# Kernel tuning notes

Hardware: AMD Instinct MI355X
Metric: run time of the kernel (lower is better)

The kernel has to match this reference:

```python
import jax, jax.numpy as jnp
import numpy as np

N_NODES = 100000
N_EDGES = 1250000
D = 64


def setup_inputs() -> dict:
    key = jax.random.key(0)
    k0, k1, k2, k3, k4 = jax.random.split(key, 5)
    feat = jax.random.normal(k0, (N_NODES, D), dtype=jnp.float32)
    src = jax.random.randint(k1, (N_EDGES,), 0, N_NODES)
    dst = jax.random.randint(k2, (N_EDGES,), 0, N_NODES)
    # GIN apply_func: Linear(D, D) -> ReLU -> Linear(D, D)
    scale = 1.0 / np.sqrt(D)
    W1 = jax.random.uniform(k3, (D, D), dtype=jnp.float32, minval=-scale, maxval=scale)
    b1 = jnp.zeros((D,), dtype=jnp.float32)
    W2 = jax.random.uniform(k4, (D, D), dtype=jnp.float32, minval=-scale, maxval=scale)
    b2 = jnp.zeros((D,), dtype=jnp.float32)
    eps = jnp.zeros((1,), dtype=jnp.float32)  # learnable eps, init 0
    return {"feat": feat, "W1": W1, "b1": b1, "W2": W2, "b2": b2,
            "eps": eps, "src": src, "dst": dst}


def reference(feat, W1, b1, W2, b2, eps, src, dst):
    # copy_u + sum reduce: gather source features per edge, scatter-add to dst
    msgs = feat[src]                                   # [E, D]
    neigh = jax.ops.segment_sum(msgs, dst, num_segments=feat.shape[0])  # [N, D]
    rst = (1.0 + eps) * feat + neigh                   # combine
    # apply_func (f_Theta): 2-layer MLP
    h = jax.nn.relu(rst @ W1 + b1)
    out = h @ W2 + b2
    return out
```

## Files before the change

### kernel.cpp

```cpp
#include <hip/hip_runtime.h>
#include <hip/hip_bf16.h>

#define N_NODES 100000
#define N_EDGES 1250000
#define DIM 64
#define NB 782
#define NCHUNK 512
#define CHUNK 2442
#define MAXE 4096

typedef __attribute__((ext_vector_type(8))) short short8;
typedef __attribute__((ext_vector_type(8))) __bf16 bf16x8;
typedef __attribute__((ext_vector_type(4))) float f32x4;

static __device__ __forceinline__ short f2bf(float f) {
    union { float f; unsigned u; } v; v.f = f;
    unsigned r = (v.u + 0x7fffu + ((v.u >> 16) & 1u)) >> 16;
    return (short)r;
}
static __device__ __forceinline__ float bfu2f(unsigned u) {
    union { unsigned u; float f; } v; v.u = u << 16; return v.f;
}
static __device__ __forceinline__ float bfs2f(short s) {
    union { unsigned u; float f; } v; v.u = ((unsigned)(unsigned short)s) << 16; return v.f;
}
static __device__ __forceinline__ int wave_scan(int v, int lane) {
#pragma unroll
    for (int off = 1; off < 64; off <<= 1) {
        int n = __shfl_up(v, off, 64);
        if (lane >= off) v += n;
    }
    return v;
}

__global__ __launch_bounds__(256) void prologue(const float* __restrict__ feat,
                                                short* __restrict__ featbf,
                                                const float* __restrict__ W1,
                                                const float* __restrict__ W2,
                                                short* __restrict__ wf,
                                                int basePrep) {
    int blk = blockIdx.x;
    if (blk < basePrep) {
        int i = (blk * 256 + threadIdx.x) * 8;
        float4 a = *(const float4*)(feat + i);
        float4 b = *(const float4*)(feat + i + 4);
        short8 t;
        t[0] = f2bf(a.x); t[1] = f2bf(a.y); t[2] = f2bf(a.z); t[3] = f2bf(a.w);
        t[4] = f2bf(b.x); t[5] = f2bf(b.y); t[6] = f2bf(b.z); t[7] = f2bf(b.w);
        *(short8*)(featbf + i) = t;
    } else {
        int idx = (blk - basePrep) * 256 + threadIdx.x;
        int layer = idx >> 12;
        int fi = idx & 4095;
        int fragidx = fi >> 9;
        int lane = (fi >> 3) & 63;
        int jj = fi & 7;
        int ct = fragidx >> 1, kt = fragidx & 1;
        int k = kt * 32 + (lane >> 4) * 8 + jj;
        int j = ct * 16 + (lane & 15);
        const float* W = layer ? W2 : W1;
        wf[idx] = f2bf(W[k * DIM + j]);
    }
}

__global__ __launch_bounds__(512) void partition3(const int* __restrict__ src,
                                                  const int* __restrict__ dst,
                                                  int* __restrict__ offs_gT,
                                                  int* __restrict__ edgebuf) {
    __shared__ int cnt[NB];
    __shared__ int lcur[NB];
    __shared__ int wsum[8];
    __shared__ int estage[CHUNK];

    int c = blockIdx.x;
    int t = threadIdx.x;
    int lane = t & 63, wv = t >> 6;
    int base = c * CHUNK;
    int end = base + CHUNK; if (end > N_EDGES) end = N_EDGES;

    for (int b = t; b < NB; b += 512) cnt[b] = 0;
    __syncthreads();
    for (int i = base + t; i < end; i += 512)
        atomicAdd(&cnt[dst[i] >> 7], 1);
    __syncthreads();

    int b0 = 2 * t, b1 = 2 * t + 1;
    int v0 = (b0 < NB) ? cnt[b0] : 0;
    int v1 = (b1 < NB) ? cnt[b1] : 0;
    int isc = wave_scan(v0 + v1, lane);
    if (lane == 63) wsum[wv] = isc;
    __syncthreads();
    if (wv == 0) {
        int s = (lane < 8) ? wsum[lane] : 0;
#pragma unroll
        for (int off = 1; off < 8; off <<= 1) {
            int n = __shfl_up(s, off, 64);
            if (lane >= off) s += n;
        }
        if (lane < 8) wsum[lane] = s;
    }
    __syncthreads();
    int ex = (wv ? wsum[wv - 1] : 0) + isc - (v0 + v1);
    if (b0 < NB) { lcur[b0] = ex;      offs_gT[(size_t)b0 * NCHUNK + c] = ex; }
    if (b1 < NB) { lcur[b1] = ex + v0; offs_gT[(size_t)b1 * NCHUNK + c] = ex + v0; }
    if (t == 511) offs_gT[(size_t)NB * NCHUNK + c] = wsum[7];
    __syncthreads();

    for (int i = base + t; i < end; i += 512) {
        int d = dst[i];
        int p = atomicAdd(&lcur[d >> 7], 1);
        estage[p] = src[i] | ((d & 127) << 17);
    }
    __syncthreads();

    int n = end - base;
    for (int i = t; i < n; i += 512) edgebuf[base + i] = estage[i];
}

template<int BF>
__global__ __launch_bounds__(512) void fused_gather_mlp(const int* __restrict__ offs_gT,
                                                        const int* __restrict__ edgebuf,
                                                        const void* __restrict__ featp,
                                                        const float* __restrict__ feat,
                                                        const short* __restrict__ wf,
                                                        const float* __restrict__ b1,
                                                        const float* __restrict__ b2,
                                                        const float* __restrict__ epsp,
                                                        float* __restrict__ out) {
    __shared__ union {
        struct { int ew[MAXE]; int es[MAXE]; } s;
        float tile[128][66];
    } u;
    __shared__ int cnt[128], offs[128], cur[128];
    __shared__ int slen[NCHUNK], dloc[NCHUNK];
    __shared__ int wsum[8];
    __shared__ int csum[2];

    int b = blockIdx.x;
    int node0 = b << 7;
    int tid = threadIdx.x;
    int lane = tid & 63, wv8 = tid >> 6;
    int c = tid & 15;
    int slot = tid >> 4;

    int s0 = offs_gT[(size_t)b * NCHUNK + tid];
    int myslen = offs_gT[(size_t)(b + 1) * NCHUNK + tid] - s0;
    int isc = wave_scan(myslen, lane);
    if (lane == 63) wsum[wv8] = isc;
    __syncthreads();
    if (wv8 == 0) {
        int s = (lane < 8) ? wsum[lane] : 0;
#pragma unroll
        for (int off = 1; off < 8; off <<= 1) {
            int n = __shfl_up(s, off, 64);
            if (lane >= off) s += n;
        }
        if (lane < 8) wsum[lane] = s;
    }
    __syncthreads();
    int incl = (wv8 ? wsum[wv8 - 1] : 0) + isc;
    dloc[tid] = incl - myslen;
    slen[tid] = myslen;
    int ec = wsum[7];
    __syncthreads();

    float acc[4][4];
#pragma unroll
    for (int g = 0; g < 4; ++g)
#pragma unroll
        for (int j = 0; j < 4; ++j) acc[g][j] = 0.f;

    int c0 = 0;
    while (c0 < NCHUNK) {
        int rbase = dloc[c0];
        int pred = (tid >= c0) && (dloc[tid] + slen[tid] - rbase <= MAXE);
        int nc = __syncthreads_count(pred);
        int c1 = c0 + nc;

        if (tid < 128) cnt[tid] = 0;
        if (tid >= c0 && tid < c1 && myslen > 0) {
            int d0 = dloc[tid] - rbase;
            const int* sp = edgebuf + (size_t)tid * CHUNK + s0;
            for (int i = 0; i < myslen; ++i) u.s.ew[d0 + i] = sp[i];
        }
        __syncthreads();

        int n = ((c1 < NCHUNK) ? dloc[c1] : ec) - rbase;

        for (int i = tid; i < n; i += 512)
            atomicAdd(&cnt[(u.s.ew[i] >> 17) & 127], 1);
        __syncthreads();

        int v_c = (tid < 128) ? cnt[tid] : 0;
        int s_c = 0;
        if (wv8 < 2) {
            s_c = wave_scan(v_c, lane);
            if (lane == 63) csum[wv8] = s_c;
        }
        __syncthreads();
        if (tid < 128) {
            int basec = (wv8 == 1) ? csum[0] : 0;
            int x = basec + s_c - v_c;
            offs[tid] = x;
            cur[tid] = x;
        }
        __syncthreads();

        for (int i = tid; i < n; i += 512) {
            int w = u.s.ew[i];
            int p = atomicAdd(&cur[(w >> 17) & 127], 1);
            u.s.es[p] = w & 0x1FFFF;
        }
        __syncthreads();

#pragma unroll
        for (int g = 0; g < 4; ++g) {
            int ld = g * 32 + slot;
            int e0 = offs[ld], e1 = e0 + cnt[ld];
            int i = e0;
            if (BF) {
                const uint2* fb = (const uint2*)featp;
                for (; i + 7 < e1; i += 8) {
                    uint2 pv[8];
#pragma unroll
                    for (int k = 0; k < 8; ++k) pv[k] = fb[u.s.es[i + k] * 16 + c];
                    float a0 = 0.f, a1 = 0.f, a2 = 0.f, a3 = 0.f;
#pragma unroll
                    for (int k = 0; k < 8; ++k) {
                        a0 += bfu2f(pv[k].x & 0xffffu);
                        a1 += bfu2f(pv[k].x >> 16);
                        a2 += bfu2f(pv[k].y & 0xffffu);
                        a3 += bfu2f(pv[k].y >> 16);
                    }
                    acc[g][0] += a0; acc[g][1] += a1;
                    acc[g][2] += a2; acc[g][3] += a3;
                }
                for (; i + 3 < e1; i += 4) {
                    uint2 pv[4];
#pragma unroll
                    for (int k = 0; k < 4; ++k) pv[k] = fb[u.s.es[i + k] * 16 + c];
#pragma unroll
                    for (int k = 0; k < 4; ++k) {
                        acc[g][0] += bfu2f(pv[k].x & 0xffffu);
                        acc[g][1] += bfu2f(pv[k].x >> 16);
                        acc[g][2] += bfu2f(pv[k].y & 0xffffu);
                        acc[g][3] += bfu2f(pv[k].y >> 16);
                    }
                }
                for (; i < e1; ++i) {
                    uint2 pa = fb[u.s.es[i] * 16 + c];
                    acc[g][0] += bfu2f(pa.x & 0xffffu);
                    acc[g][1] += bfu2f(pa.x >> 16);
                    acc[g][2] += bfu2f(pa.y & 0xffffu);
                    acc[g][3] += bfu2f(pa.y >> 16);
                }
            } else {
                const float4* ff = (const float4*)featp;
                for (; i + 3 < e1; i += 4) {
                    float4 pv[4];
#pragma unroll
                    for (int k = 0; k < 4; ++k) pv[k] = ff[u.s.es[i + k] * 16 + c];
#pragma unroll
                    for (int k = 0; k < 4; ++k) {
                        acc[g][0] += pv[k].x; acc[g][1] += pv[k].y;
                        acc[g][2] += pv[k].z; acc[g][3] += pv[k].w;
                    }
                }
                for (; i < e1; ++i) {
                    float4 qa = ff[u.s.es[i] * 16 + c];
                    acc[g][0] += qa.x; acc[g][1] += qa.y;
                    acc[g][2] += qa.z; acc[g][3] += qa.w;
                }
            }
        }
        __syncthreads();
        c0 = c1;
    }

#pragma unroll
    for (int g = 0; g < 4; ++g) {
        int ld = g * 32 + slot;
#pragma unroll
        for (int j = 0; j < 4; ++j)
            u.tile[ld][c * 4 + j] = acc[g][j];
    }
    __syncthreads();

    int r = lane & 15, gg = lane >> 4;
    int lrow = wv8 * 16 + r;
    int node = node0 + lrow;
    bool valid = node < N_NODES;
    float epsv = 1.0f + epsp[0];

    const short8* w1f8 = (const short8*)(wf);
    const short8* w2f8 = (const short8*)(wf + 4096);

    short8 a[2];
#pragma unroll
    for (int kt = 0; kt < 2; ++kt) {
        float fv[8];
        if (BF) {
            short8 f8 = { 0,0,0,0,0,0,0,0 };
            if (valid) f8 = ((const short8*)featp)[node * 8 + kt * 4 + gg];
#pragma unroll
            for (int jj = 0; jj < 8; ++jj) fv[jj] = bfs2f(f8[jj]);
        } else {
            float4 f0 = { 0,0,0,0 }, f1 = { 0,0,0,0 };
            if (valid) {
                const float* fp = feat + (size_t)node * 64 + kt * 32 + gg * 8;
                f0 = *(const float4*)fp;
                f1 = *(const float4*)(fp + 4);
            }
            fv[0]=f0.x; fv[1]=f0.y; fv[2]=f0.z; fv[3]=f0.w;
            fv[4]=f1.x; fv[5]=f1.y; fv[6]=f1.z; fv[7]=f1.w;
        }
        const float2* tp = (const float2*)&u.tile[lrow][kt * 32 + gg * 8];
        float2 n0 = tp[0], n1 = tp[1], n2 = tp[2], n3 = tp[3];
        float rs[8] = { epsv * fv[0] + n0.x, epsv * fv[1] + n0.y,
                        epsv * fv[2] + n1.x, epsv * fv[3] + n1.y,
                        epsv * fv[4] + n2.x, epsv * fv[5] + n2.y,
                        epsv * fv[6] + n3.x, epsv * fv[7] + n3.y };
        short8 t;
#pragma unroll
        for (int jj = 0; jj < 8; ++jj) t[jj] = f2bf(rs[jj]);
        a[kt] = t;
    }
    __syncthreads();

    f32x4 acc1[4];
#pragma unroll
    for (int ct = 0; ct < 4; ++ct) {
        float bv = b1[ct * 16 + r];
        f32x4 cc = { bv, bv, bv, bv };
        cc = __builtin_amdgcn_mfma_f32_16x16x32_bf16(
                __builtin_bit_cast(bf16x8, a[0]),
                __builtin_bit_cast(bf16x8, w1f8[(ct * 2 + 0) * 64 + lane]),
                cc, 0, 0, 0);
        cc = __builtin_amdgcn_mfma_f32_16x16x32_bf16(
                __builtin_bit_cast(bf16x8, a[1]),
                __builtin_bit_cast(bf16x8, w1f8[(ct * 2 + 1) * 64 + lane]),
                cc, 0, 0, 0);
        acc1[ct] = cc;
    }

#pragma unroll
    for (int ct = 0; ct < 4; ++ct)
#pragma unroll
        for (int i = 0; i < 4; ++i)
            u.tile[wv8 * 16 + gg * 4 + i][ct * 16 + r] = fmaxf(acc1[ct][i], 0.0f);
    __syncthreads();

    short8 a2[2];
#pragma unroll
    for (int kt = 0; kt < 2; ++kt) {
        const float2* hp = (const float2*)&u.tile[wv8 * 16 + r][kt * 32 + gg * 8];
        float2 h0 = hp[0], h1 = hp[1], h2 = hp[2], h3 = hp[3];
        float hs[8] = { h0.x, h0.y, h1.x, h1.y, h2.x, h2.y, h3.x, h3.y };
        short8 t;
#pragma unroll
        for (int jj = 0; jj < 8; ++jj) t[jj] = f2bf(hs[jj]);
        a2[kt] = t;
    }

    f32x4 acc2[4];
#pragma unroll
    for (int ct = 0; ct < 4; ++ct) {
        float bv = b2[ct * 16 + r];
        f32x4 cc = { bv, bv, bv, bv };
        cc = __builtin_amdgcn_mfma_f32_16x16x32_bf16(
                __builtin_bit_cast(bf16x8, a2[0]),
                __builtin_bit_cast(bf16x8, w2f8[(ct * 2 + 0) * 64 + lane]),
                cc, 0, 0, 0);
        cc = __builtin_amdgcn_mfma_f32_16x16x32_bf16(
                __builtin_bit_cast(bf16x8, a2[1]),
                __builtin_bit_cast(bf16x8, w2f8[(ct * 2 + 1) * 64 + lane]),
                cc, 0, 0, 0);
        acc2[ct] = cc;
    }

#pragma unroll
    for (int ct = 0; ct < 4; ++ct)
#pragma unroll
        for (int i = 0; i < 4; ++i) {
            int nrow = node0 + wv8 * 16 + gg * 4 + i;
            if (nrow < N_NODES)
                out[(size_t)nrow * 64 + ct * 16 + r] = acc2[ct][i];
        }
}

__global__ __launch_bounds__(256) void scatter_edges(const float4* __restrict__ feat4,
                                                     const int* __restrict__ src,
                                                     const int* __restrict__ dst,
                                                     float* __restrict__ neigh) {
    int idx = blockIdx.x * 256 + threadIdx.x;
    int e = idx >> 4, c = idx & 15;
    int s = src[e], d = dst[e];
    float4 v = feat4[s * 16 + c];
    float* p = neigh + d * 64 + c * 4;
    unsafeAtomicAdd(p + 0, v.x);
    unsafeAtomicAdd(p + 1, v.y);
    unsafeAtomicAdd(p + 2, v.z);
    unsafeAtomicAdd(p + 3, v.w);
}

__global__ __launch_bounds__(256) void prep_w(const float* __restrict__ W1,
                                              const float* __restrict__ W2,
                                              short* __restrict__ wf) {
    int idx = blockIdx.x * 256 + threadIdx.x;
    int layer = idx >> 12;
    int fi = idx & 4095;
    int fragidx = fi >> 9;
    int lane = (fi >> 3) & 63;
    int jj = fi & 7;
    int ct = fragidx >> 1, kt = fragidx & 1;
    int k = kt * 32 + (lane >> 4) * 8 + jj;
    int j = ct * 16 + (lane & 15);
    const float* W = layer ? W2 : W1;
    wf[idx] = f2bf(W[k * DIM + j]);
}

__global__ __launch_bounds__(256) void gin_mlp(const float* __restrict__ feat,
                                               float* __restrict__ neigh_out,
                                               const short* __restrict__ wf,
                                               const float* __restrict__ b1,
                                               const float* __restrict__ b2,
                                               const float* __restrict__ epsp) {
    __shared__ float hbuf[4][16][66];
    int lane = threadIdx.x & 63;
    int wv = threadIdx.x >> 6;
    int r = lane & 15, g = lane >> 4;
    int row0 = blockIdx.x * 64 + wv * 16;
    int node = row0 + r;
    bool valid = node < N_NODES;
    float epsv = 1.0f + epsp[0];
    const short8* w1f8 = (const short8*)(wf);
    const short8* w2f8 = (const short8*)(wf + 4096);
    short8 a[2];
    if (valid) {
        const float* fp = feat + node * 64 + g * 8;
        const float* np_ = neigh_out + node * 64 + g * 8;
#pragma unroll
        for (int kt = 0; kt < 2; ++kt) {
            float4 f0 = *(const float4*)(fp + kt * 32);
            float4 f1 = *(const float4*)(fp + kt * 32 + 4);
            float4 n0 = *(const float4*)(np_ + kt * 32);
            float4 n1 = *(const float4*)(np_ + kt * 32 + 4);
            float rs[8] = { epsv * f0.x + n0.x, epsv * f0.y + n0.y,
                            epsv * f0.z + n0.z, epsv * f0.w + n0.w,
                            epsv * f1.x + n1.x, epsv * f1.y + n1.y,
                            epsv * f1.z + n1.z, epsv * f1.w + n1.w };
            short8 t;
#pragma unroll
            for (int jj = 0; jj < 8; ++jj) t[jj] = f2bf(rs[jj]);
            a[kt] = t;
        }
    } else {
        short8 z = { 0,0,0,0,0,0,0,0 };
        a[0] = z; a[1] = z;
    }
    f32x4 acc[4];
#pragma unroll
    for (int ct = 0; ct < 4; ++ct) {
        float bv = b1[ct * 16 + r];
        f32x4 c = { bv, bv, bv, bv };
        c = __builtin_amdgcn_mfma_f32_16x16x32_bf16(
                __builtin_bit_cast(bf16x8, a[0]),
                __builtin_bit_cast(bf16x8, w1f8[(ct * 2 + 0) * 64 + lane]), c, 0, 0, 0);
        c = __builtin_amdgcn_mfma_f32_16x16x32_bf16(
                __builtin_bit_cast(bf16x8, a[1]),
                __builtin_bit_cast(bf16x8, w1f8[(ct * 2 + 1) * 64 + lane]), c, 0, 0, 0);
        acc[ct] = c;
    }
#pragma unroll
    for (int ct = 0; ct < 4; ++ct)
#pragma unroll
        for (int i = 0; i < 4; ++i)
            hbuf[wv][g * 4 + i][ct * 16 + r] = fmaxf(acc[ct][i], 0.0f);
    __syncthreads();
    short8 a2[2];
#pragma unroll
    for (int kt = 0; kt < 2; ++kt) {
        const float2* hp = (const float2*)&hbuf[wv][r][kt * 32 + g * 8];
        float2 h0 = hp[0], h1 = hp[1], h2 = hp[2], h3 = hp[3];
        float hs[8] = { h0.x, h0.y, h1.x, h1.y, h2.x, h2.y, h3.x, h3.y };
        short8 t;
#pragma unroll
        for (int jj = 0; jj < 8; ++jj) t[jj] = f2bf(hs[jj]);
        a2[kt] = t;
    }
    f32x4 acc2[4];
#pragma unroll
    for (int ct = 0; ct < 4; ++ct) {
        float bv = b2[ct * 16 + r];
        f32x4 c = { bv, bv, bv, bv };
        c = __builtin_amdgcn_mfma_f32_16x16x32_bf16(
                __builtin_bit_cast(bf16x8, a2[0]),
                __builtin_bit_cast(bf16x8, w2f8[(ct * 2 + 0) * 64 + lane]), c, 0, 0, 0);
        c = __builtin_amdgcn_mfma_f32_16x16x32_bf16(
                __builtin_bit_cast(bf16x8, a2[1]),
                __builtin_bit_cast(bf16x8, w2f8[(ct * 2 + 1) * 64 + lane]), c, 0, 0, 0);
        acc2[ct] = c;
    }
#pragma unroll
    for (int ct = 0; ct < 4; ++ct)
#pragma unroll
        for (int i = 0; i < 4; ++i) {
            int nrow = row0 + g * 4 + i;
            if (nrow < N_NODES)
                neigh_out[nrow * 64 + ct * 16 + r] = acc2[ct][i];
        }
}

extern "C" void kernel_launch(void* const* d_in, const int* in_sizes, int n_in,
                              void* d_out, int out_size, void* d_ws, size_t ws_size,
                              hipStream_t stream) {
    const float* feat = (const float*)d_in[0];
    const float* W1   = (const float*)d_in[1];
    const float* b1   = (const float*)d_in[2];
    const float* W2   = (const float*)d_in[3];
    const float* b2   = (const float*)d_in[4];
    const float* eps  = (const float*)d_in[5];
    const int*   src  = (const int*)d_in[6];
    const int*   dst  = (const int*)d_in[7];
    float* out = (float*)d_out;

    char* ws = (char*)d_ws;
    short* wf = (short*)ws;

    const size_t featbf_bytes = (size_t)N_NODES * DIM * 2;
    const size_t offs_bytes   = (size_t)(NB + 1) * NCHUNK * 4;
    const size_t edge_bytes   = (size_t)NCHUNK * CHUNK * 4;
    const size_t need_mid  = 16384 + offs_bytes + edge_bytes;
    const size_t need_full = need_mid + featbf_bytes;

    if (ws_size >= need_mid) {
        char* p = ws + 16384;
        short* featbf = nullptr;
        if (ws_size >= need_full) { featbf = (short*)p; p += featbf_bytes; }
        int* offs_gT = (int*)p;            p += offs_bytes;
        int* edgebuf = (int*)p;

        int basePrep = featbf ? 3125 : 0;
        prologue<<<basePrep + 32, 256, 0, stream>>>(feat, featbf, W1, W2, wf, basePrep);

        partition3<<<NCHUNK, 512, 0, stream>>>(src, dst, offs_gT, edgebuf);

        if (featbf)
            fused_gather_mlp<1><<<NB, 512, 0, stream>>>(
                offs_gT, edgebuf, featbf, feat, wf, b1, b2, eps, out);
        else
            fused_gather_mlp<0><<<NB, 512, 0, stream>>>(
                offs_gT, edgebuf, feat, feat, wf, b1, b2, eps, out);
    } else {
        prep_w<<<32, 256, 0, stream>>>(W1, W2, wf);
        hipMemsetAsync(d_out, 0, (size_t)N_NODES * DIM * sizeof(float), stream);
        scatter_edges<<<(N_EDGES * 16) / 256, 256, 0, stream>>>(
            (const float4*)feat, src, dst, out);
        gin_mlp<<<(N_NODES + 63) / 64, 256, 0, stream>>>(feat, out, wf, b1, b2, eps);
    }
}
```

Before: 71.20 us.

## Store partition offsets chunk-major and simplify bf16 gather unpacking

The per-chunk bucket offsets are now stored chunk-major, one row of NB+1 entries per chunk, instead of bucket-major. Partition writes become contiguous per block, while each gather block now reads strided entries (stride NB+1) across 512 rows. The bf16 gather loop drops the 8-wide unrolled path, keeping a 4-wide path that loads four rows and sums them directly into the accumulators. The high half of each packed value is extracted with a mask instead of a shift, saving an ALU op per element. Fewer loads are in flight per thread, which may reduce memory-level parallelism in the gather.

```diff
diff --git a/kernel.cpp b/kernel.cpp
--- a/kernel.cpp
+++ b/kernel.cpp
@@ -18,8 +18,11 @@
     unsigned r = (v.u + 0x7fffu + ((v.u >> 16) & 1u)) >> 16;
     return (short)r;
 }
-static __device__ __forceinline__ float bfu2f(unsigned u) {
+static __device__ __forceinline__ float bflo(unsigned u) {
     union { unsigned u; float f; } v; v.u = u << 16; return v.f;
+}
+static __device__ __forceinline__ float bfhi(unsigned u) {
+    union { unsigned u; float f; } v; v.u = u & 0xffff0000u; return v.f;
 }
 static __device__ __forceinline__ float bfs2f(short s) {
     union { unsigned u; float f; } v; v.u = ((unsigned)(unsigned short)s) << 16; return v.f;
@@ -65,7 +68,7 @@
 
 __global__ __launch_bounds__(512) void partition3(const int* __restrict__ src,
                                                   const int* __restrict__ dst,
-                                                  int* __restrict__ offs_gT,
+                                                  int* __restrict__ offs_g,
                                                   int* __restrict__ edgebuf) {
     __shared__ int cnt[NB];
     __shared__ int lcur[NB];
@@ -101,9 +104,10 @@
     }
     __syncthreads();
     int ex = (wv ? wsum[wv - 1] : 0) + isc - (v0 + v1);
-    if (b0 < NB) { lcur[b0] = ex;      offs_gT[(size_t)b0 * NCHUNK + c] = ex; }
-    if (b1 < NB) { lcur[b1] = ex + v0; offs_gT[(size_t)b1 * NCHUNK + c] = ex + v0; }
-    if (t == 511) offs_gT[(size_t)NB * NCHUNK + c] = wsum[7];
+    int* orow = offs_g + (size_t)c * (NB + 1);
+    if (b0 < NB) { lcur[b0] = ex;      orow[b0] = ex; }
+    if (b1 < NB) { lcur[b1] = ex + v0; orow[b1] = ex + v0; }
+    if (t == 511) orow[NB] = wsum[7];
     __syncthreads();
 
     for (int i = base + t; i < end; i += 512) {
@@ -118,7 +122,7 @@
 }
 
 template<int BF>
-__global__ __launch_bounds__(512) void fused_gather_mlp(const int* __restrict__ offs_gT,
+__global__ __launch_bounds__(512) void fused_gather_mlp(const int* __restrict__ offs_g,
                                                         const int* __restrict__ edgebuf,
                                                         const void* __restrict__ featp,
                                                         const float* __restrict__ feat,
@@ -143,8 +147,9 @@
     int c = tid & 15;
     int slot = tid >> 4;
 
-    int s0 = offs_gT[(size_t)b * NCHUNK + tid];
-    int myslen = offs_gT[(size_t)(b + 1) * NCHUNK + tid] - s0;
+    const int* row = offs_g + (size_t)tid * (NB + 1);
+    int s0 = row[b];
+    int myslen = row[b + 1] - s0;
     int isc = wave_scan(myslen, lane);
     if (lane == 63) wsum[wv8] = isc;
     __syncthreads();
@@ -220,39 +225,22 @@
             int i = e0;
             if (BF) {
                 const uint2* fb = (const uint2*)featp;
-                for (; i + 7 < e1; i += 8) {
-                    uint2 pv[8];
-#pragma unroll
-                    for (int k = 0; k < 8; ++k) pv[k] = fb[u.s.es[i + k] * 16 + c];
-                    float a0 = 0.f, a1 = 0.f, a2 = 0.f, a3 = 0.f;
-#pragma unroll
-                    for (int k = 0; k < 8; ++k) {
-                        a0 += bfu2f(pv[k].x & 0xffffu);
-                        a1 += bfu2f(pv[k].x >> 16);
-                        a2 += bfu2f(pv[k].y & 0xffffu);
-                        a3 += bfu2f(pv[k].y >> 16);
-                    }
-                    acc[g][0] += a0; acc[g][1] += a1;
-                    acc[g][2] += a2; acc[g][3] += a3;
-                }
                 for (; i + 3 < e1; i += 4) {
-                    uint2 pv[4];
-#pragma unroll
-                    for (int k = 0; k < 4; ++k) pv[k] = fb[u.s.es[i + k] * 16 + c];
-#pragma unroll
-                    for (int k = 0; k < 4; ++k) {
-                        acc[g][0] += bfu2f(pv[k].x & 0xffffu);
-                        acc[g][1] += bfu2f(pv[k].x >> 16);
-                        acc[g][2] += bfu2f(pv[k].y & 0xffffu);
-                        acc[g][3] += bfu2f(pv[k].y >> 16);
-                    }
+                    int sa = u.s.es[i], sb = u.s.es[i + 1];
+                    int sc_ = u.s.es[i + 2], sd = u.s.es[i + 3];
+                    uint2 p0 = fb[sa * 16 + c];
+                    uint2 p1 = fb[sb * 16 + c];
+                    uint2 p2 = fb[sc_ * 16 + c];
+                    uint2 p3 = fb[sd * 16 + c];
+                    acc[g][0] += bflo(p0.x) + bflo(p1.x) + bflo(p2.x) + bflo(p3.x);
+                    acc[g][1] += bfhi(p0.x) + bfhi(p1.x) + bfhi(p2.x) + bfhi(p3.x);
+                    acc[g][2] += bflo(p0.y) + bflo(p1.y) + bflo(p2.y) + bflo(p3.y);
+                    acc[g][3] += bfhi(p0.y) + bfhi(p1.y) + bfhi(p2.y) + bfhi(p3.y);
                 }
                 for (; i < e1; ++i) {
                     uint2 pa = fb[u.s.es[i] * 16 + c];
-                    acc[g][0] += bfu2f(pa.x & 0xffffu);
-                    acc[g][1] += bfu2f(pa.x >> 16);
-                    acc[g][2] += bfu2f(pa.y & 0xffffu);
-                    acc[g][3] += bfu2f(pa.y >> 16);
+                    acc[g][0] += bflo(pa.x); acc[g][1] += bfhi(pa.x);
+                    acc[g][2] += bflo(pa.y); acc[g][3] += bfhi(pa.y);
                 }
             } else {
                 const float4* ff = (const float4*)featp;
@@ -528,7 +516,7 @@
     short* wf = (short*)ws;
 
     const size_t featbf_bytes = (size_t)N_NODES * DIM * 2;
-    const size_t offs_bytes   = (size_t)(NB + 1) * NCHUNK * 4;
+    const size_t offs_bytes   = (size_t)NCHUNK * (NB + 1) * 4;
     const size_t edge_bytes   = (size_t)NCHUNK * CHUNK * 4;
     const size_t need_mid  = 16384 + offs_bytes + edge_bytes;
     const size_t need_full = need_mid + featbf_bytes;
@@ -537,20 +525,20 @@
         char* p = ws + 16384;
         short* featbf = nullptr;
         if (ws_size >= need_full) { featbf = (short*)p; p += featbf_bytes; }
-        int* offs_gT = (int*)p;            p += offs_bytes;
+        int* offs_g  = (int*)p;            p += offs_bytes;
         int* edgebuf = (int*)p;
 
         int basePrep = featbf ? 3125 : 0;
         prologue<<<basePrep + 32, 256, 0, stream>>>(feat, featbf, W1, W2, wf, basePrep);
 
-        partition3<<<NCHUNK, 512, 0, stream>>>(src, dst, offs_gT, edgebuf);
+        partition3<<<NCHUNK, 512, 0, stream>>>(src, dst, offs_g, edgebuf);
 
         if (featbf)
             fused_gather_mlp<1><<<NB, 512, 0, stream>>>(
-                offs_gT, edgebuf, featbf, feat, wf, b1, b2, eps, out);
+                offs_g, edgebuf, featbf, feat, wf, b1, b2, eps, out);
         else
             fused_gather_mlp<0><<<NB, 512, 0, stream>>>(
-                offs_gT, edgebuf, feat, feat, wf, b1, b2, eps, out);
+                offs_g, edgebuf, feat, feat, wf, b1, b2, eps, out);
     } else {
         prep_w<<<32, 256, 0, stream>>>(W1, W2, wf);
         hipMemsetAsync(d_out, 0, (size_t)N_NODES * DIM * sizeof(float), stream);
```

Measured after the change: 71.87 us. Within noise of the previous version (+0.9%).
